# Kernel tuning notes

Hardware: AMD Instinct MI355X
Metric: run time of the kernel (lower is better)

## Reference

```python
import jax, jax.numpy as jnp
import numpy as np

N = 50000          # residues
E = 1000000        # edges
H = 128            # hidden_channels
CUT = 11.5         # cutoff
NR = 6             # num_radial
NS = 3             # num_spherical
NPE = 16           # num_pos_emb

def swish(x):
    return x * jax.nn.sigmoid(x)

def rbf(d):
    # Bessel-style radial basis with smooth cosine cutoff, [E, NR]
    u = jnp.clip(d / CUT, 0.0, 1.0)
    n = jnp.arange(1, NR + 1, dtype=jnp.float32)
    fc = 0.5 * (jnp.cos(jnp.pi * u) + 1.0)
    return jnp.sqrt(2.0 / CUT) * jnp.sin(n * jnp.pi * u[:, None]) / (d[:, None] + 1e-6) * fc[:, None]

def angle_emb(d, ang):
    # d_angle_emb: radial x cos(l*angle) -> [E, NR*NS]
    r = rbf(d)
    l = jnp.arange(NS, dtype=jnp.float32)
    a = jnp.cos(ang[:, None] * l)
    return (r[:, :, None] * a[:, None, :]).reshape(d.shape[0], NR * NS)

def theta_phi_emb(d, theta, phi):
    # d_theta_phi_emb: radial x angular(theta) x angular(phi) -> [E, NR*NS*NS]
    r = rbf(d)
    l = jnp.arange(NS, dtype=jnp.float32)
    ct = jnp.cos(theta[:, None] * l)
    cp = jnp.cos(phi[:, None] * l)
    return jnp.einsum('en,el,em->enlm', r, ct, cp).reshape(d.shape[0], NR * NS * NS)


def setup_inputs():
    key = jax.random.key(0)
    ks = jax.random.split(key, 20)
    f32 = jnp.float32
    pos = jax.random.normal(ks[0], (N, 3), f32) * 8.0
    pos_n = pos + jax.random.normal(ks[1], (N, 3), f32) * 0.8
    pos_c = pos + jax.random.normal(ks[2], (N, 3), f32) * 0.8
    z = jax.random.randint(ks[3], (N,), 0, 26)
    bb_embs = jax.random.normal(ks[4], (N, 6), f32)
    side_chain_embs = jax.random.normal(ks[5], (N, 8), f32)
    esm_embs = jax.random.normal(ks[6], (N, 1280), f32)
    batch = jnp.zeros((N,), jnp.int32)
    edge_index = jax.random.randint(ks[7], (2, E), 0, N)
    def w(k, shape):
        return jax.random.normal(k, shape, f32) * (1.0 / np.sqrt(shape[0]))
    edge_in = NR * NS * NS + 3 * NR * NS + NPE  # 54 + 54 + 16 = 124
    params = dict(
        W_emb=w(ks[8], (26 + 6 + 8, H // 2)), b_emb=jnp.zeros((H // 2,), f32),
        W_esm=w(ks[9], (1280, H // 2)), b_esm=jnp.zeros((H // 2,), f32),
        W_edge=w(ks[10], (edge_in, H)),
        W_msg=w(ks[11], (H, H)),
        W_upd=w(ks[12], (H, H)),
        W_o0=w(ks[13], (H, H)), b_o0=jnp.zeros((H,), f32),
        W_o1=w(ks[14], (H, 32)), b_o1=jnp.zeros((32,), f32),
        W_of=w(ks[15], (32, 1)), b_of=jnp.zeros((1,), f32),
        W_n0=w(ks[16], (H, 32)), b_n0=jnp.zeros((32,), f32),
        W_nf=w(ks[17], (32, 2)), b_nf=jnp.zeros((2,), f32),
    )
    return dict(z=z, pos=pos, pos_n=pos_n, pos_c=pos_c, bb_embs=bb_embs,
                side_chain_embs=side_chain_embs, esm_embs=esm_embs,
                batch=batch, edge_index=edge_index, **params)


def reference(z, pos, pos_n, pos_c, bb_embs, side_chain_embs, esm_embs, batch,
              edge_index, W_emb, b_emb, W_esm, b_esm, W_edge, W_msg, W_upd,
              W_o0, b_o0, W_o1, b_o1, W_of, b_of, W_n0, b_n0, W_nf, b_nf):
    # --- node embedding fusion (level='allatom+esm') ---
    oh = jax.nn.one_hot(z, 26, dtype=jnp.float32)
    x_a = jnp.concatenate([oh, bb_embs, side_chain_embs], axis=1) @ W_emb + b_emb
    x_s = esm_embs @ W_esm + b_esm
    x = jnp.concatenate([x_a, x_s], axis=-1)  # [N, H]

    j, i = edge_index[0], edge_index[1]

    # --- sinusoidal positional embedding of sequence offsets ---
    dpe = (j - i).astype(jnp.float32)
    freq = jnp.exp(jnp.arange(0, NPE, 2, dtype=jnp.float32) * (-np.log(10000.0) / NPE))
    ang = dpe[:, None] * freq
    pe = jnp.concatenate([jnp.cos(ang), jnp.sin(ang)], axis=-1)  # [E, NPE]

    # --- distance / theta / phi (triplet gathers via sequence neighbors) ---
    v_ji = pos[j] - pos[i]
    dist = jnp.linalg.norm(pos[i] - pos[j], axis=1)
    refi0 = (i - 1) % N
    refi1 = (i + 1) % N
    v_r0 = pos[refi0] - pos[i]
    v_r1 = pos[refi1] - pos[i]
    a = jnp.sum(v_ji * v_r0, axis=-1)
    b = jnp.linalg.norm(jnp.cross(v_ji, v_r0), axis=-1)
    theta = jnp.arctan2(b, a)
    p1 = jnp.cross(v_r0, v_r1)
    p2 = jnp.cross(v_r0, v_ji)
    a = jnp.sum(p1 * p2, axis=-1)
    b = jnp.sum(jnp.cross(p1, p2) * v_r0, axis=-1) / (jnp.linalg.norm(v_r0, axis=-1) + 1e-7)
    phi = jnp.arctan2(b, a)
    feature0 = theta_phi_emb(dist, theta, phi)  # [E, 54]

    # --- backbone-frame Euler angles (allatom branch) ---
    o1x = pos_n[i] - pos[i]
    o1z = jnp.cross(o1x, jnp.cross(o1x, pos_c[i] - pos[i]))
    o1zl = jnp.linalg.norm(o1z, axis=1) + 1e-7
    o2x = pos_n[j] - pos[j]
    o2z = jnp.cross(o2x, jnp.cross(o2x, pos_c[j] - pos[j]))
    o2zl = jnp.linalg.norm(o2z, axis=1) + 1e-7
    nvec = jnp.cross(o1z, o2z)
    angle1 = jnp.arctan2(jnp.sum(jnp.cross(o1x, nvec) * o1z, -1) / o1zl, jnp.sum(o1x * nvec, -1))
    angle2 = jnp.arctan2(jnp.linalg.norm(nvec, axis=-1), jnp.sum(o1z * o2z, -1))
    angle3 = jnp.arctan2(jnp.sum(jnp.cross(nvec, o2x) * o2z, -1) / o2zl, jnp.sum(nvec * o2x, -1))
    feature1 = jnp.concatenate([angle_emb(dist, angle1), angle_emb(dist, angle2),
                                angle_emb(dist, angle3)], axis=1)  # [E, 54]

    # --- message passing (gather-compute-scatter stand-in for model_E) ---
    ef = swish(jnp.concatenate([feature0, feature1, pe], axis=-1) @ W_edge)  # [E, H]
    m = swish(x[j] @ W_msg) * ef
    agg = jax.ops.segment_sum(m, i, num_segments=N)
    xe = x + swish(agg @ W_upd)

    # --- output heads (dropout inactive at inference) ---
    xn = jax.nn.relu(x @ W_n0 + b_n0)
    node_out = xn @ W_nf + b_nf                   # [N, 2]
    h = jax.nn.relu(xe @ W_o0 + b_o0)
    h = jax.nn.relu(h @ W_o1 + b_o1)
    out = jax.nn.sigmoid(h @ W_of + b_of)         # [N, 1]
    return out, node_out
```

## Files before the change

### kernel.cpp

```cpp
#include <hip/hip_runtime.h>
#include <math.h>
#include <stdint.h>

#define NRES 50000
#define NEDGE 1000000
#define PI_F 3.14159265358979323846f
#define NSEG 196

typedef __attribute__((ext_vector_type(8))) short short8;
typedef __attribute__((ext_vector_type(4))) float floatx4;
typedef __attribute__((ext_vector_type(2))) short bf16x2;
typedef __attribute__((address_space(1))) bf16x2* gbf16x2p;

struct f3 { float x, y, z; };
__device__ __forceinline__ f3 ld3(const float* __restrict__ p, int i) {
  return {p[3*i+0], p[3*i+1], p[3*i+2]};
}
__device__ __forceinline__ f3 f3sub(f3 a, f3 b){ return {a.x-b.x, a.y-b.y, a.z-b.z}; }
__device__ __forceinline__ f3 f3cross(f3 a, f3 b){
  return {a.y*b.z - a.z*b.y, a.z*b.x - a.x*b.z, a.x*b.y - a.y*b.x};
}
__device__ __forceinline__ float f3dot(f3 a, f3 b){ return a.x*b.x + a.y*b.y + a.z*b.z; }
__device__ __forceinline__ float swish_fast(float v){
  return v * __builtin_amdgcn_rcpf(1.0f + __expf(-v));
}
__device__ __forceinline__ short f2bf(float f){
  unsigned u = __float_as_uint(f);
  unsigned r = (u + 0x7fffu + ((u >> 16) & 1u)) >> 16;
  return (short)r;
}
__device__ __forceinline__ float bf2f(short s){
  return __uint_as_float(((unsigned)(unsigned short)s) << 16);
}
__device__ __forceinline__ float cos_atan2(float y, float x){
  return x * __builtin_amdgcn_rsqf(fmaxf(x*x + y*y, 1e-30f));
}
__device__ __forceinline__ void atom_pk_bf16(short* addr, bf16x2 v){
  __builtin_amdgcn_global_atomic_fadd_v2bf16((gbf16x2p)(uintptr_t)addr, v);
}

__device__ __forceinline__ void edge_features(
    int e, int j, int i,
    const float* __restrict__ pos, const float* __restrict__ posn,
    const float* __restrict__ posc, short (*sF)[136])
{
  f3 pj = ld3(pos, j), pi = ld3(pos, i);
  f3 vji = f3sub(pj, pi);
  float nji2 = f3dot(vji, vji);
  float dist = sqrtf(nji2);
  int r0i = (i == 0) ? (NRES - 1) : (i - 1);
  int r1i = (i == NRES - 1) ? 0 : (i + 1);
  f3 vr0 = f3sub(ld3(pos, r0i), pi);
  f3 vr1 = f3sub(ld3(pos, r1i), pi);
  float nr02 = f3dot(vr0, vr0);

  float ct = f3dot(vji, vr0) * __builtin_amdgcn_rsqf(fmaxf(nji2 * nr02, 1e-30f));
  f3 p1 = f3cross(vr0, vr1);
  f3 p2 = f3cross(vr0, vji);
  float pa = f3dot(p1, p2);
  float pb = f3dot(f3cross(p1, p2), vr0) / (sqrtf(nr02) + 1e-7f);
  float cp = cos_atan2(pb, pa);

  f3 pni = ld3(posn, i), pci = ld3(posc, i);
  f3 o1x = f3sub(pni, pi);
  f3 o1z = f3cross(o1x, f3cross(o1x, f3sub(pci, pi)));
  float no1z2 = f3dot(o1z, o1z);
  float o1zl = sqrtf(no1z2) + 1e-7f;
  f3 pnj = ld3(posn, j), pcj = ld3(posc, j);
  f3 o2x = f3sub(pnj, pj);
  f3 o2z = f3cross(o2x, f3cross(o2x, f3sub(pcj, pj)));
  float no2z2 = f3dot(o2z, o2z);
  float o2zl = sqrtf(no2z2) + 1e-7f;
  f3 nv = f3cross(o1z, o2z);
  float y1 = f3dot(f3cross(o1x, nv), o1z) / o1zl;
  float ca1 = cos_atan2(y1, f3dot(o1x, nv));
  float ca2 = f3dot(o1z, o2z) * __builtin_amdgcn_rsqf(fmaxf(no1z2 * no2z2, 1e-30f));
  float y3 = f3dot(f3cross(nv, o2x), o2z) / o2zl;
  float ca3 = cos_atan2(y3, f3dot(nv, o2x));

  float u = fminf(dist * (1.0f/11.5f), 1.0f);
  float spu, cpu;
  __sincosf(PI_F * u, &spu, &cpu);
  float fc = 0.5f * (cpu + 1.0f);
  float pref = 0.41702882811414954f * __builtin_amdgcn_rcpf(dist + 1e-6f) * fc;
  float rb[6];
  {
    float twoc = 2.0f * cpu;
    float s_nm1 = 0.0f, s_n = spu;
    #pragma unroll
    for (int nn = 0; nn < 6; ++nn) {
      rb[nn] = pref * s_n;
      float s_np1 = twoc * s_n - s_nm1;
      s_nm1 = s_n; s_n = s_np1;
    }
  }

  float ctv[3] = {1.0f, ct, 2.0f*ct*ct - 1.0f};
  float cpv[3] = {1.0f, cp, 2.0f*cp*cp - 1.0f};
  #pragma unroll
  for (int nn = 0; nn < 6; ++nn)
    #pragma unroll
    for (int l = 0; l < 3; ++l)
      #pragma unroll
      for (int m = 0; m < 3; ++m)
        sF[e][nn*9 + l*3 + m] = f2bf(rb[nn] * ctv[l] * cpv[m]);

  float cas[3] = {ca1, ca2, ca3};
  #pragma unroll
  for (int t = 0; t < 3; ++t) {
    float c = cas[t];
    float cav[3] = {1.0f, c, 2.0f*c*c - 1.0f};
    #pragma unroll
    for (int nn = 0; nn < 6; ++nn)
      #pragma unroll
      for (int l = 0; l < 3; ++l)
        sF[e][54 + t*18 + nn*3 + l] = f2bf(rb[nn] * cav[l]);
  }

  const float FRQ[8] = {1.0f, 0.31622776601683794f, 0.1f, 0.03162277660168379f,
                        0.01f, 0.003162277660168379f, 0.001f, 0.0003162277660168379f};
  float dpe = (float)(j - i);
  #pragma unroll
  for (int q = 0; q < 8; ++q) {
    float s, c;
    __sincosf(dpe * FRQ[q], &s, &c);
    sF[e][108 + q] = f2bf(c);
    sF[e][116 + q] = f2bf(s);
  }
  sF[e][124] = 0; sF[e][125] = 0; sF[e][126] = 0; sF[e][127] = 0;
}

__global__ __launch_bounds__(256) void k_wprep(
    const float* __restrict__ We, const float* __restrict__ Wm,
    const float* __restrict__ Ws, const float* __restrict__ Wu,
    const float* __restrict__ Wo0, const float* __restrict__ Wn0,
    const float* __restrict__ Wo1,
    short* __restrict__ Wef, short* __restrict__ Wmf, short* __restrict__ Wsf,
    short* __restrict__ Wuf, short* __restrict__ Wo0f,
    short* __restrict__ Wn0f, short* __restrict__ Wo1f)
{
  int gid = blockIdx.x * 256 + threadIdx.x;
  const float* src; short* dst; int NT, K, N, t;
  if      (gid < 16384)  { t = gid;          src = We;  dst = Wef;  NT = 8; K = 124;  N = 128; }
  else if (gid < 32768)  { t = gid - 16384;  src = Wm;  dst = Wmf;  NT = 8; K = 128;  N = 128; }
  else if (gid < 114688) { t = gid - 32768;  src = Ws;  dst = Wsf;  NT = 4; K = 1280; N = 64;  }
  else if (gid < 131072) { t = gid - 114688; src = Wu;  dst = Wuf;  NT = 8; K = 128;  N = 128; }
  else if (gid < 147456) { t = gid - 131072; src = Wo0; dst = Wo0f; NT = 8; K = 128;  N = 128; }
  else if (gid < 151552) { t = gid - 147456; src = Wn0; dst = Wn0f; NT = 2; K = 128;  N = 32;  }
  else if (gid < 155648) { t = gid - 151552; src = Wo1; dst = Wo1f; NT = 2; K = 128;  N = 32;  }
  else return;
  int j = t & 7, lane = (t >> 3) & 63;
  int rest = t >> 9;
  int nt = rest % NT, kt = rest / NT;
  int k = kt*32 + (lane >> 4)*8 + j, n = nt*16 + (lane & 15);
  dst[t] = f2bf((k < K) ? src[k*N + n] : 0.0f);
}

__global__ __launch_bounds__(256) void k_hist(
    const int* __restrict__ ei, int* __restrict__ bins)
{
  int e = blockIdx.x * 256 + threadIdx.x;
  if (e < NEDGE) atomicAdd(&bins[ei[NEDGE + e]], 1);
}

__global__ __launch_bounds__(256) void k_scan1(
    int* __restrict__ bins, int* __restrict__ bsum)
{
  __shared__ int s[256];
  const int t = threadIdx.x, b = blockIdx.x;
  const int idx = b * 256 + t;
  int v = (idx < NRES) ? bins[idx] : 0;
  s[t] = v;
  __syncthreads();
  #pragma unroll
  for (int d = 1; d < 256; d <<= 1) {
    int add = (t >= d) ? s[t - d] : 0;
    __syncthreads();
    if (t >= d) s[t] += add;
    __syncthreads();
  }
  if (idx < NRES) bins[idx] = s[t] - v;
  if (t == 255) bsum[b] = s[255];
}

__global__ __launch_bounds__(256) void k_scan2(int* __restrict__ bsum)
{
  __shared__ int s[256];
  const int t = threadIdx.x;
  int v = (t < NSEG) ? bsum[t] : 0;
  s[t] = v;
  __syncthreads();
  #pragma unroll
  for (int d = 1; d < 256; d <<= 1) {
    int add = (t >= d) ? s[t - d] : 0;
    __syncthreads();
    if (t >= d) s[t] += add;
    __syncthreads();
  }
  if (t < NSEG) bsum[t] = s[t] - v;
}

__global__ __launch_bounds__(256) void k_scan3(
    int* __restrict__ bins, const int* __restrict__ bsum)
{
  int idx = blockIdx.x * 256 + threadIdx.x;
  if (idx < NRES) bins[idx] += bsum[blockIdx.x];
}

__global__ __launch_bounds__(256) void k_scatter(
    const int* __restrict__ ei, int* __restrict__ bins, int* __restrict__ perm)
{
  int e = blockIdx.x * 256 + threadIdx.x;
  if (e < NEDGE) {
    int i = ei[NEDGE + e];
    int slot = atomicAdd(&bins[i], 1);
    if (slot >= 0 && slot < NEDGE) perm[slot] = e;
  }
}

__global__ __launch_bounds__(256) void k_xa(
    const int* __restrict__ z, const float* __restrict__ bb,
    const float* __restrict__ side, const float* __restrict__ W_emb,
    const float* __restrict__ b_emb, short* __restrict__ xb)
{
  int tid = threadIdx.x;
  int h = tid & 63;
  int n = blockIdx.x * 4 + (tid >> 6);
  if (n >= NRES) return;
  int zz = z[n];
  float acc = W_emb[zz * 64 + h] + b_emb[h];
  #pragma unroll
  for (int k = 0; k < 6; ++k) acc += bb[n*6 + k] * W_emb[(26 + k)*64 + h];
  #pragma unroll
  for (int k = 0; k < 8; ++k) acc += side[n*8 + k] * W_emb[(32 + k)*64 + h];
  xb[(size_t)n * 128 + h] = f2bf(acc);
}

__global__ __launch_bounds__(256) void k_esm(
    const float* __restrict__ esm, const short* __restrict__ Wsf,
    const float* __restrict__ b, short* __restrict__ xb)
{
  const int tid = threadIdx.x;
  const int lane = tid & 63, w = tid >> 6;
  const int quad = lane >> 4, colb = lane & 15;
  const int tile0 = blockIdx.x * 64 + w * 16;

  int arow = tile0 + colb;
  if (arow >= NRES) arow = NRES - 1;
  const float* ap = esm + (size_t)arow * 1280 + quad * 8;

  floatx4 acc[4];
  #pragma unroll
  for (int nt = 0; nt < 4; ++nt) acc[nt] = (floatx4){0.f, 0.f, 0.f, 0.f};

  for (int kt = 0; kt < 40; ++kt) {
    float4 v0 = *(const float4*)(ap + kt*32);
    float4 v1 = *(const float4*)(ap + kt*32 + 4);
    short8 a;
    a[0] = f2bf(v0.x); a[1] = f2bf(v0.y); a[2] = f2bf(v0.z); a[3] = f2bf(v0.w);
    a[4] = f2bf(v1.x); a[5] = f2bf(v1.y); a[6] = f2bf(v1.z); a[7] = f2bf(v1.w);
    #pragma unroll
    for (int nt = 0; nt < 4; ++nt) {
      short8 bf = *(const short8*)&Wsf[(size_t)((kt*4 + nt)*64 + lane)*8];
      acc[nt] = __builtin_amdgcn_mfma_f32_16x16x32_bf16(a, bf, acc[nt], 0, 0, 0);
    }
  }
  #pragma unroll
  for (int nt = 0; nt < 4; ++nt) {
    int ch = nt*16 + colb;
    float bias = b[ch];
    #pragma unroll
    for (int r = 0; r < 4; ++r) {
      int n = tile0 + quad*4 + r;
      if (n < NRES) xb[(size_t)n * 128 + 64 + ch] = f2bf(acc[nt][r] + bias);
    }
  }
}

__global__ __launch_bounds__(256) void k_msg(
    const short* __restrict__ xb, const short* __restrict__ Wmf,
    short* __restrict__ xmb)
{
  __shared__ __align__(16) short sX[64][136];
  __shared__ __align__(16) short sO[64][136];
  const int tid = threadIdx.x;
  const int lane = tid & 63, w = tid >> 6;
  const int quad = lane >> 4, colb = lane & 15;
  const int n0 = blockIdx.x * 64;

  #pragma unroll
  for (int it = 0; it < 4; ++it) {
    int idx = it * 256 + tid;
    int row = idx >> 4, c8 = idx & 15;
    int n = n0 + row;
    short8 v = (short8)(short)0;
    if (n < NRES) v = *(const short8*)&xb[(size_t)n * 128 + c8*8];
    *(short8*)&sX[row][c8*8] = v;
  }
  __syncthreads();

  floatx4 acc[4][2];
  #pragma unroll
  for (int mt = 0; mt < 4; ++mt) {
    acc[mt][0] = (floatx4){0.f,0.f,0.f,0.f};
    acc[mt][1] = (floatx4){0.f,0.f,0.f,0.f};
  }
  #pragma unroll
  for (int kt = 0; kt < 4; ++kt) {
    short8 b0 = *(const short8*)&Wmf[(size_t)((kt*8 + w*2 + 0)*64 + lane)*8];
    short8 b1 = *(const short8*)&Wmf[(size_t)((kt*8 + w*2 + 1)*64 + lane)*8];
    #pragma unroll
    for (int mt = 0; mt < 4; ++mt) {
      short8 a = *(const short8*)&sX[mt*16 + colb][kt*32 + quad*8];
      acc[mt][0] = __builtin_amdgcn_mfma_f32_16x16x32_bf16(a, b0, acc[mt][0], 0, 0, 0);
      acc[mt][1] = __builtin_amdgcn_mfma_f32_16x16x32_bf16(a, b1, acc[mt][1], 0, 0, 0);
    }
  }
  #pragma unroll
  for (int mt = 0; mt < 4; ++mt)
    #pragma unroll
    for (int nt = 0; nt < 2; ++nt)
      #pragma unroll
      for (int r = 0; r < 4; ++r)
        sO[mt*16 + quad*4 + r][w*32 + nt*16 + colb] = f2bf(swish_fast(acc[mt][nt][r]));
  __syncthreads();
  #pragma unroll
  for (int it = 0; it < 4; ++it) {
    int idx = it * 256 + tid;
    int row = idx >> 4, c8 = idx & 15;
    int n = n0 + row;
    if (n < NRES) *(short8*)&xmb[(size_t)n * 128 + c8*8] = *(short8*)&sO[row][c8*8];
  }
}

__global__ __launch_bounds__(256, 4) void k_edge_s(
    const int* __restrict__ perm, const int* __restrict__ ei,
    const float* __restrict__ pos,
    const float* __restrict__ posn, const float* __restrict__ posc,
    const short* __restrict__ xmb, const short* __restrict__ Wef,
    short* __restrict__ aggb)
{
  __shared__ int sJ[64];
  __shared__ int sI[64];
  __shared__ __align__(16) short sF[64][136];
  __shared__ __align__(16) short sXJ[64][136];

  const int tid = threadIdx.x;
  const int orig = blockIdx.x;
  const int xcd = orig & 7, sub = orig >> 3;
  const int wg = (xcd == 0 ? 0 : 1954 + (xcd - 1) * 1953) + sub;
  const int e0 = wg * 64;

  if (tid < 64) {
    int ep = perm[e0 + tid];
    ep = (ep < 0) ? 0 : ((ep >= NEDGE) ? NEDGE - 1 : ep);
    int jj = ei[ep], ii = ei[NEDGE + ep];
    sJ[tid] = (jj < 0) ? 0 : ((jj >= NRES) ? NRES - 1 : jj);
    sI[tid] = (ii < 0) ? 0 : ((ii >= NRES) ? NRES - 1 : ii);
  }
  __syncthreads();

  if (tid < 64) {
    edge_features(tid, sJ[tid], sI[tid], pos, posn, posc, sF);
  } else {
    const int t2 = tid - 64;
    for (int it = 0; it < 6; ++it) {
      int idx = it * 192 + t2;
      if (idx < 1024) {
        int row = idx >> 4;
        int c8 = idx & 15;
        *(short8*)&sXJ[row][c8*8] = *(const short8*)&xmb[(size_t)sJ[row] * 128 + c8*8];
      }
    }
  }
  __syncthreads();

  const int lane = tid & 63, w = tid >> 6;
  const int quad = lane >> 4, colb = lane & 15;
  const int nb = w * 2;

  short8 bE[4][2];
  #pragma unroll
  for (int kt = 0; kt < 4; ++kt)
    #pragma unroll
    for (int nt = 0; nt < 2; ++nt)
      bE[kt][nt] = *(const short8*)&Wef[(size_t)((kt*8 + nb + nt)*64 + lane)*8];

  floatx4 accE[4][2];
  #pragma unroll
  for (int mt = 0; mt < 4; ++mt) {
    accE[mt][0] = (floatx4){0.f, 0.f, 0.f, 0.f};
    accE[mt][1] = (floatx4){0.f, 0.f, 0.f, 0.f};
  }

  #pragma unroll
  for (int kt = 0; kt < 4; ++kt) {
    #pragma unroll
    for (int mt = 0; mt < 4; ++mt) {
      short8 af = *(const short8*)&sF[mt*16 + colb][kt*32 + quad*8];
      #pragma unroll
      for (int nt = 0; nt < 2; ++nt)
        accE[mt][nt] = __builtin_amdgcn_mfma_f32_16x16x32_bf16(af, bE[kt][nt], accE[mt][nt], 0, 0, 0);
    }
  }
  __syncthreads();

  short (*sM)[136] = sF;
  #pragma unroll
  for (int mt = 0; mt < 4; ++mt)
    #pragma unroll
    for (int nt = 0; nt < 2; ++nt) {
      int ch = w*32 + nt*16 + colb;
      #pragma unroll
      for (int r = 0; r < 4; ++r) {
        int e = mt*16 + quad*4 + r;
        float mv = bf2f(sXJ[e][ch]) * swish_fast(accE[mt][nt][r]);
        sM[e][ch] = f2bf(mv);
      }
    }
  __syncthreads();

  {
    const int p = tid & 63;
    const int g = tid >> 6;
    float ax = 0.f, ay = 0.f;
    int cur = sI[g * 16];
    #pragma unroll
    for (int rr = 0; rr < 16; ++rr) {
      int row = g * 16 + rr;
      int ii = sI[row];
      if (ii != cur) {
        bf16x2 v; v[0] = f2bf(ax); v[1] = f2bf(ay);
        atom_pk_bf16(&aggb[(size_t)cur * 128 + p*2], v);
        ax = 0.f; ay = 0.f; cur = ii;
      }
      bf16x2 mv = *(const bf16x2*)&sM[row][p*2];
      ax += bf2f(mv[0]); ay += bf2f(mv[1]);
    }
    bf16x2 v; v[0] = f2bf(ax); v[1] = f2bf(ay);
    atom_pk_bf16(&aggb[(size_t)cur * 128 + p*2], v);
  }
}

__global__ __launch_bounds__(256, 4) void k_edge_b(
    const int* __restrict__ ei, const float* __restrict__ pos,
    const float* __restrict__ posn, const float* __restrict__ posc,
    const short* __restrict__ xb, const short* __restrict__ Wef,
    const short* __restrict__ Wmf, short* __restrict__ aggb)
{
  __shared__ int sJ[64];
  __shared__ int sI[64];
  __shared__ __align__(16) short sF[64][136];
  __shared__ __align__(16) short sXJ[64][136];

  const int tid = threadIdx.x;
  const int e0 = blockIdx.x * 64;

  if (tid < 64) { sJ[tid] = ei[e0 + tid]; sI[tid] = ei[NEDGE + e0 + tid]; }
  __syncthreads();

  if (tid < 64) {
    edge_features(tid, sJ[tid], sI[tid], pos, posn, posc, sF);
  } else {
    const int t2 = tid - 64;
    for (int it = 0; it < 6; ++it) {
      int idx = it * 192 + t2;
      if (idx < 1024) {
        int row = idx >> 4;
        int c8 = idx & 15;
        *(short8*)&sXJ[row][c8*8] = *(const short8*)&xb[(size_t)sJ[row] * 128 + c8*8];
      }
    }
  }
  __syncthreads();

  const int lane = tid & 63, w = tid >> 6;
  const int quad = lane >> 4, colb = lane & 15;
  const int nb = w * 2;

  short8 bE[4][2], bM[4][2];
  #pragma unroll
  for (int kt = 0; kt < 4; ++kt)
    #pragma unroll
    for (int nt = 0; nt < 2; ++nt) {
      bE[kt][nt] = *(const short8*)&Wef[(size_t)((kt*8 + nb + nt)*64 + lane)*8];
      bM[kt][nt] = *(const short8*)&Wmf[(size_t)((kt*8 + nb + nt)*64 + lane)*8];
    }

  floatx4 accE[4][2], accM[4][2];
  #pragma unroll
  for (int mt = 0; mt < 4; ++mt)
    #pragma unroll
    for (int nt = 0; nt < 2; ++nt) {
      accE[mt][nt] = (floatx4){0.f, 0.f, 0.f, 0.f};
      accM[mt][nt] = (floatx4){0.f, 0.f, 0.f, 0.f};
    }

  #pragma unroll
  for (int kt = 0; kt < 4; ++kt) {
    #pragma unroll
    for (int mt = 0; mt < 4; ++mt) {
      short8 af = *(const short8*)&sF [mt*16 + colb][kt*32 + quad*8];
      short8 ax = *(const short8*)&sXJ[mt*16 + colb][kt*32 + quad*8];
      #pragma unroll
      for (int nt = 0; nt < 2; ++nt) {
        accE[mt][nt] = __builtin_amdgcn_mfma_f32_16x16x32_bf16(af, bE[kt][nt], accE[mt][nt], 0, 0, 0);
        accM[mt][nt] = __builtin_amdgcn_mfma_f32_16x16x32_bf16(ax, bM[kt][nt], accM[mt][nt], 0, 0, 0);
      }
    }
  }
  __syncthreads();

  short (*sM)[136] = sXJ;
  #pragma unroll
  for (int mt = 0; mt < 4; ++mt)
    #pragma unroll
    for (int nt = 0; nt < 2; ++nt) {
      int ch = w*32 + nt*16 + colb;
      #pragma unroll
      for (int r = 0; r < 4; ++r) {
        int e = mt*16 + quad*4 + r;
        sM[e][ch] = f2bf(swish_fast(accM[mt][nt][r]) * swish_fast(accE[mt][nt][r]));
      }
    }
  __syncthreads();

  #pragma unroll
  for (int it = 0; it < 16; ++it) {
    int flat = it * 256 + tid;
    int row = flat >> 6, p = flat & 63;
    bf16x2 v = *(const bf16x2*)&sM[row][p*2];
    atom_pk_bf16(&aggb[(size_t)sI[row] * 128 + p*2], v);
  }
}

__global__ __launch_bounds__(256) void k_upd(
    const short* __restrict__ xb, const short* __restrict__ aggb,
    const short* __restrict__ Wuf, const short* __restrict__ Wo0f,
    const short* __restrict__ Wn0f, const short* __restrict__ Wo1f,
    const float* __restrict__ bn0, const float* __restrict__ Wnf,
    const float* __restrict__ bnf, const float* __restrict__ bo0,
    const float* __restrict__ bo1, const float* __restrict__ Wof,
    const float* __restrict__ bof, float* __restrict__ out0,
    float* __restrict__ out1)
{
  __shared__ __align__(16) short sA[64][136];
  __shared__ __align__(16) short sX[64][136];
  __shared__ float sS[64][33];

  const int tid = threadIdx.x;
  const int lane = tid & 63, w = tid >> 6;
  const int quad = lane >> 4, colb = lane & 15;
  const int n0 = blockIdx.x * 64;

  #pragma unroll
  for (int it = 0; it < 4; ++it) {
    int idx = it * 256 + tid;
    int row = idx >> 4, c8 = idx & 15;
    int n = n0 + row;
    short8 va = (short8)(short)0, vx = (short8)(short)0;
    if (n < NRES) {
      va = *(const short8*)&aggb[(size_t)n * 128 + c8*8];
      vx = *(const short8*)&xb  [(size_t)n * 128 + c8*8];
    }
    *(short8*)&sA[row][c8*8] = va;
    *(short8*)&sX[row][c8*8] = vx;
  }
  __syncthreads();

  {
    floatx4 accN[2];
    accN[0] = (floatx4){0.f,0.f,0.f,0.f}; accN[1] = (floatx4){0.f,0.f,0.f,0.f};
    #pragma unroll
    for (int kt = 0; kt < 4; ++kt) {
      short8 a = *(const short8*)&sX[w*16 + colb][kt*32 + quad*8];
      #pragma unroll
      for (int nt = 0; nt < 2; ++nt) {
        short8 bf = *(const short8*)&Wn0f[(size_t)((kt*2 + nt)*64 + lane)*8];
        accN[nt] = __builtin_amdgcn_mfma_f32_16x16x32_bf16(a, bf, accN[nt], 0, 0, 0);
      }
    }
    #pragma unroll
    for (int nt = 0; nt < 2; ++nt) {
      int col = nt*16 + colb;
      float bias = bn0[col];
      #pragma unroll
      for (int r = 0; r < 4; ++r)
        sS[w*16 + quad*4 + r][col] = fmaxf(accN[nt][r] + bias, 0.0f);
    }
  }
  __syncthreads();
  if (tid < 128) {
    int row = tid >> 1, oc = tid & 1;
    int n = n0 + row;
    if (n < NRES) {
      float a2 = bnf[oc];
      #pragma unroll
      for (int k = 0; k < 32; ++k) a2 += sS[row][k] * Wnf[k*2 + oc];
      out1[(size_t)n * 2 + oc] = a2;
    }
  }

  floatx4 acc1[4][2];
  #pragma unroll
  for (int mt = 0; mt < 4; ++mt) {
    acc1[mt][0] = (floatx4){0.f,0.f,0.f,0.f};
    acc1[mt][1] = (floatx4){0.f,0.f,0.f,0.f};
  }
  #pragma unroll
  for (int kt = 0; kt < 4; ++kt) {
    short8 b0 = *(const short8*)&Wuf[(size_t)((kt*8 + w*2 + 0)*64 + lane)*8];
    short8 b1 = *(const short8*)&Wuf[(size_t)((kt*8 + w*2 + 1)*64 + lane)*8];
    #pragma unroll
    for (int mt = 0; mt < 4; ++mt) {
      short8 a = *(const short8*)&sA[mt*16 + colb][kt*32 + quad*8];
      acc1[mt][0] = __builtin_amdgcn_mfma_f32_16x16x32_bf16(a, b0, acc1[mt][0], 0, 0, 0);
      acc1[mt][1] = __builtin_amdgcn_mfma_f32_16x16x32_bf16(a, b1, acc1[mt][1], 0, 0, 0);
    }
  }
  __syncthreads();
  #pragma unroll
  for (int mt = 0; mt < 4; ++mt)
    #pragma unroll
    for (int nt = 0; nt < 2; ++nt)
      #pragma unroll
      for (int r = 0; r < 4; ++r) {
        int row = mt*16 + quad*4 + r, col = w*32 + nt*16 + colb;
        float xv = bf2f(sX[row][col]);
        sA[row][col] = f2bf(xv + swish_fast(acc1[mt][nt][r]));
      }
  __syncthreads();

  floatx4 acc2[4][2];
  #pragma unroll
  for (int mt = 0; mt < 4; ++mt) {
    acc2[mt][0] = (floatx4){0.f,0.f,0.f,0.f};
    acc2[mt][1] = (floatx4){0.f,0.f,0.f,0.f};
  }
  #pragma unroll
  for (int kt = 0; kt < 4; ++kt) {
    short8 b0 = *(const short8*)&Wo0f[(size_t)((kt*8 + w*2 + 0)*64 + lane)*8];
    short8 b1 = *(const short8*)&Wo0f[(size_t)((kt*8 + w*2 + 1)*64 + lane)*8];
    #pragma unroll
    for (int mt = 0; mt < 4; ++mt) {
      short8 a = *(const short8*)&sA[mt*16 + colb][kt*32 + quad*8];
      acc2[mt][0] = __builtin_amdgcn_mfma_f32_16x16x32_bf16(a, b0, acc2[mt][0], 0, 0, 0);
      acc2[mt][1] = __builtin_amdgcn_mfma_f32_16x16x32_bf16(a, b1, acc2[mt][1], 0, 0, 0);
    }
  }
  __syncthreads();
  #pragma unroll
  for (int mt = 0; mt < 4; ++mt)
    #pragma unroll
    for (int nt = 0; nt < 2; ++nt) {
      int col = w*32 + nt*16 + colb;
      float bias = bo0[col];
      #pragma unroll
      for (int r = 0; r < 4; ++r) {
        int row = mt*16 + quad*4 + r;
        sX[row][col] = f2bf(fmaxf(acc2[mt][nt][r] + bias, 0.0f));
      }
    }
  __syncthreads();

  {
    floatx4 accH[2];
    accH[0] = (floatx4){0.f,0.f,0.f,0.f}; accH[1] = (floatx4){0.f,0.f,0.f,0.f};
    #pragma unroll
    for (int kt = 0; kt < 4; ++kt) {
      short8 a = *(const short8*)&sX[w*16 + colb][kt*32 + quad*8];
      #pragma unroll
      for (int nt = 0; nt < 2; ++nt) {
        short8 bf = *(const short8*)&Wo1f[(size_t)((kt*2 + nt)*64 + lane)*8];
        accH[nt] = __builtin_amdgcn_mfma_f32_16x16x32_bf16(a, bf, accH[nt], 0, 0, 0);
      }
    }
    __syncthreads();
    #pragma unroll
    for (int nt = 0; nt < 2; ++nt) {
      int col = nt*16 + colb;
      float bias = bo1[col];
      #pragma unroll
      for (int r = 0; r < 4; ++r)
        sS[w*16 + quad*4 + r][col] = fmaxf(accH[nt][r] + bias, 0.0f);
    }
  }
  __syncthreads();

  if (tid < 64) {
    int n = n0 + tid;
    if (n < NRES) {
      float a2 = bof[0];
      #pragma unroll
      for (int k = 0; k < 32; ++k) a2 += sS[tid][k] * Wof[k];
      out0[n] = 1.0f / (1.0f + expf(-a2));
    }
  }
}

extern "C" void kernel_launch(void* const* d_in, const int* in_sizes, int n_in,
                              void* d_out, int out_size, void* d_ws, size_t ws_size,
                              hipStream_t stream) {
  (void)in_sizes; (void)n_in; (void)out_size;
  const int*   z     = (const int*)  d_in[0];
  const float* pos   = (const float*)d_in[1];
  const float* posn  = (const float*)d_in[2];
  const float* posc  = (const float*)d_in[3];
  const float* bb    = (const float*)d_in[4];
  const float* side  = (const float*)d_in[5];
  const float* esm   = (const float*)d_in[6];
  const int*   ei    = (const int*)  d_in[8];
  const float* W_emb = (const float*)d_in[9];
  const float* b_emb = (const float*)d_in[10];
  const float* W_esm = (const float*)d_in[11];
  const float* b_esm = (const float*)d_in[12];
  const float* W_edge= (const float*)d_in[13];
  const float* W_msg = (const float*)d_in[14];
  const float* W_upd = (const float*)d_in[15];
  const float* W_o0  = (const float*)d_in[16];
  const float* b_o0  = (const float*)d_in[17];
  const float* W_o1  = (const float*)d_in[18];
  const float* b_o1  = (const float*)d_in[19];
  const float* W_of  = (const float*)d_in[20];
  const float* b_of  = (const float*)d_in[21];
  const float* W_n0  = (const float*)d_in[22];
  const float* b_n0  = (const float*)d_in[23];
  const float* W_nf  = (const float*)d_in[24];
  const float* b_nf  = (const float*)d_in[25];

  float* out0 = (float*)d_out;
  float* out1 = out0 + NRES;
  char* ws = (char*)d_ws;

  const bool full = (ws_size >= (size_t)42912096);

  if (full) {
    short* xb   = (short*)ws;
    short* aggb = (short*)(ws + 12800000);
    short* xmb  = (short*)(ws + 25600000);
    short* Wef  = (short*)(ws + 38400000);
    short* Wmf  = (short*)(ws + 38432768);
    short* Wsf  = (short*)(ws + 38465536);
    short* Wuf  = (short*)(ws + 38629376);
    short* Wo0f = (short*)(ws + 38662144);
    short* Wn0f = (short*)(ws + 38694912);
    short* Wo1f = (short*)(ws + 38703104);
    int*   bins = (int*)  (ws + 38711296);
    int*   bsum = (int*)  (ws + 38911296);
    int*   perm = (int*)  (ws + 38912096);

    hipMemsetAsync(aggb, 0, (size_t)NRES * 128 * sizeof(short), stream);
    hipMemsetAsync(bins, 0, (size_t)NRES * sizeof(int), stream);

    k_wprep  <<<608, 256, 0, stream>>>(W_edge, W_msg, W_esm, W_upd, W_o0, W_n0, W_o1,
                                       Wef, Wmf, Wsf, Wuf, Wo0f, Wn0f, Wo1f);
    k_hist   <<<3907, 256, 0, stream>>>(ei, bins);
    k_scan1  <<<NSEG, 256, 0, stream>>>(bins, bsum);
    k_scan2  <<<1,    256, 0, stream>>>(bsum);
    k_scan3  <<<NSEG, 256, 0, stream>>>(bins, bsum);
    k_scatter<<<3907, 256, 0, stream>>>(ei, bins, perm);
    k_xa     <<<12500, 256, 0, stream>>>(z, bb, side, W_emb, b_emb, xb);
    k_esm    <<<782,   256, 0, stream>>>(esm, Wsf, b_esm, xb);
    k_msg    <<<782,   256, 0, stream>>>(xb, Wmf, xmb);
    k_edge_s <<<15625, 256, 0, stream>>>(perm, ei, pos, posn, posc, xmb, Wef, aggb);
    k_upd    <<<782,   256, 0, stream>>>(xb, aggb, Wuf, Wo0f, Wn0f, Wo1f,
                                         b_n0, W_nf, b_nf, b_o0, b_o1, W_of, b_of,
                                         out0, out1);
  } else {
    short* xb   = (short*)ws;
    short* aggb = (short*)(ws + 12800000);
    short* Wef  = (short*)(ws + 25600000);
    short* Wmf  = (short*)(ws + 25632768);
    short* Wsf  = (short*)(ws + 25665536);
    short* Wuf  = (short*)(ws + 25829376);
    short* Wo0f = (short*)(ws + 25862144);
    short* Wn0f = (short*)(ws + 25894912);
    short* Wo1f = (short*)(ws + 25903104);

    hipMemsetAsync(aggb, 0, (size_t)NRES * 128 * sizeof(short), stream);

    k_wprep <<<608, 256, 0, stream>>>(W_edge, W_msg, W_esm, W_upd, W_o0, W_n0, W_o1,
                                      Wef, Wmf, Wsf, Wuf, Wo0f, Wn0f, Wo1f);
    k_xa    <<<12500, 256, 0, stream>>>(z, bb, side, W_emb, b_emb, xb);
    k_esm   <<<782,   256, 0, stream>>>(esm, Wsf, b_esm, xb);
    k_edge_b<<<15625, 256, 0, stream>>>(ei, pos, posn, posc, xb, Wef, Wmf, aggb);
    k_upd   <<<782,   256, 0, stream>>>(xb, aggb, Wuf, Wo0f, Wn0f, Wo1f,
                                        b_n0, W_nf, b_nf, b_o0, b_o1, W_of, b_of,
                                        out0, out1);
  }
}
```

Measured before the change: 728.5 us.

## Fuse node embedding, ESM projection and message GEMM; store sorted edge pairs

Merges the three node kernels (atom embedding, ESM projection, message GEMM) into one k_node kernel that keeps the assembled x tile in shared memory instead of writing xb and reading it back. The scatter step now writes (j,i) pairs directly in sorted order, so the edge kernel no longer does a dependent gather through perm into edge_index. Edge-feature bf16 stores are packed two at a time with v_cvt_pk_bf16_f32. The workspace threshold for the full path rises by 4 MB, which may send smaller workspaces to the fallback path.

```diff
diff --git a/kernel.cpp b/kernel.cpp
--- a/kernel.cpp
+++ b/kernel.cpp
@@ -37,6 +37,11 @@
 }
 __device__ __forceinline__ void atom_pk_bf16(short* addr, bf16x2 v){
   __builtin_amdgcn_global_atomic_fadd_v2bf16((gbf16x2p)(uintptr_t)addr, v);
+}
+__device__ __forceinline__ unsigned pkbf(float lo, float hi){
+  unsigned r;
+  asm("v_cvt_pk_bf16_f32 %0, %1, %2" : "=v"(r) : "v"(lo), "v"(hi));
+  return r;
 }
 
 __device__ __forceinline__ void edge_features(
@@ -95,6 +100,7 @@
     }
   }
 
+  float pend = 0.0f;
   float ctv[3] = {1.0f, ct, 2.0f*ct*ct - 1.0f};
   float cpv[3] = {1.0f, cp, 2.0f*cp*cp - 1.0f};
   #pragma unroll
@@ -102,8 +108,12 @@
     #pragma unroll
     for (int l = 0; l < 3; ++l)
       #pragma unroll
-      for (int m = 0; m < 3; ++m)
-        sF[e][nn*9 + l*3 + m] = f2bf(rb[nn] * ctv[l] * cpv[m]);
+      for (int m = 0; m < 3; ++m) {
+        const int f = nn*9 + l*3 + m;
+        float v = rb[nn] * ctv[l] * cpv[m];
+        if (f & 1) *(unsigned*)&sF[e][f-1] = pkbf(pend, v);
+        else       pend = v;
+      }
 
   float cas[3] = {ca1, ca2, ca3};
   #pragma unroll
@@ -113,21 +123,27 @@
     #pragma unroll
     for (int nn = 0; nn < 6; ++nn)
       #pragma unroll
-      for (int l = 0; l < 3; ++l)
-        sF[e][54 + t*18 + nn*3 + l] = f2bf(rb[nn] * cav[l]);
+      for (int l = 0; l < 3; ++l) {
+        const int f = 54 + t*18 + nn*3 + l;
+        float v = rb[nn] * cav[l];
+        if (f & 1) *(unsigned*)&sF[e][f-1] = pkbf(pend, v);
+        else       pend = v;
+      }
   }
 
   const float FRQ[8] = {1.0f, 0.31622776601683794f, 0.1f, 0.03162277660168379f,
                         0.01f, 0.003162277660168379f, 0.001f, 0.0003162277660168379f};
   float dpe = (float)(j - i);
-  #pragma unroll
-  for (int q = 0; q < 8; ++q) {
-    float s, c;
-    __sincosf(dpe * FRQ[q], &s, &c);
-    sF[e][108 + q] = f2bf(c);
-    sF[e][116 + q] = f2bf(s);
-  }
-  sF[e][124] = 0; sF[e][125] = 0; sF[e][126] = 0; sF[e][127] = 0;
+  float cb[8], sb[8];
+  #pragma unroll
+  for (int q = 0; q < 8; ++q) __sincosf(dpe * FRQ[q], &sb[q], &cb[q]);
+  #pragma unroll
+  for (int q = 0; q < 8; q += 2) {
+    *(unsigned*)&sF[e][108 + q] = pkbf(cb[q], cb[q+1]);
+    *(unsigned*)&sF[e][116 + q] = pkbf(sb[q], sb[q+1]);
+  }
+  *(unsigned*)&sF[e][124] = 0u;
+  *(unsigned*)&sF[e][126] = 0u;
 }
 
 __global__ __launch_bounds__(256) void k_wprep(
@@ -208,13 +224,13 @@
 }
 
 __global__ __launch_bounds__(256) void k_scatter(
-    const int* __restrict__ ei, int* __restrict__ bins, int* __restrict__ perm)
+    const int* __restrict__ ei, int* __restrict__ bins, int2* __restrict__ sij)
 {
   int e = blockIdx.x * 256 + threadIdx.x;
   if (e < NEDGE) {
-    int i = ei[NEDGE + e];
+    int j = ei[e], i = ei[NEDGE + e];
     int slot = atomicAdd(&bins[i], 1);
-    if (slot >= 0 && slot < NEDGE) perm[slot] = e;
+    if (slot >= 0 && slot < NEDGE) sij[slot] = make_int2(j, i);
   }
 }
 
@@ -277,33 +293,93 @@
   }
 }
 
-__global__ __launch_bounds__(256) void k_msg(
-    const short* __restrict__ xb, const short* __restrict__ Wmf,
-    short* __restrict__ xmb)
+__global__ __launch_bounds__(256) void k_node(
+    const float* __restrict__ esm, const short* __restrict__ Wsf,
+    const float* __restrict__ b_esm,
+    const int* __restrict__ z, const float* __restrict__ bb,
+    const float* __restrict__ side, const float* __restrict__ W_emb,
+    const float* __restrict__ b_emb,
+    const short* __restrict__ Wmf,
+    short* __restrict__ xb, short* __restrict__ xmb)
 {
   __shared__ __align__(16) short sX[64][136];
-  __shared__ __align__(16) short sO[64][136];
+
   const int tid = threadIdx.x;
   const int lane = tid & 63, w = tid >> 6;
   const int quad = lane >> 4, colb = lane & 15;
   const int n0 = blockIdx.x * 64;
+  const int tile0 = n0 + w * 16;
+
+  int arow = tile0 + colb;
+  if (arow >= NRES) arow = NRES - 1;
+  const float* ap = esm + (size_t)arow * 1280 + quad * 8;
+
+  floatx4 acc[4];
+  #pragma unroll
+  for (int nt = 0; nt < 4; ++nt) acc[nt] = (floatx4){0.f, 0.f, 0.f, 0.f};
+
+  for (int kt = 0; kt < 40; ++kt) {
+    float4 v0 = *(const float4*)(ap + kt*32);
+    float4 v1 = *(const float4*)(ap + kt*32 + 4);
+    short8 a;
+    a[0] = f2bf(v0.x); a[1] = f2bf(v0.y); a[2] = f2bf(v0.z); a[3] = f2bf(v0.w);
+    a[4] = f2bf(v1.x); a[5] = f2bf(v1.y); a[6] = f2bf(v1.z); a[7] = f2bf(v1.w);
+    #pragma unroll
+    for (int nt = 0; nt < 4; ++nt) {
+      short8 bf = *(const short8*)&Wsf[(size_t)((kt*4 + nt)*64 + lane)*8];
+      acc[nt] = __builtin_amdgcn_mfma_f32_16x16x32_bf16(a, bf, acc[nt], 0, 0, 0);
+    }
+  }
+
+  #pragma unroll
+  for (int nt = 0; nt < 4; ++nt) {
+    int ch = nt*16 + colb;
+    float bias = b_esm[ch];
+    #pragma unroll
+    for (int r = 0; r < 4; ++r)
+      sX[w*16 + quad*4 + r][64 + ch] = f2bf(acc[nt][r] + bias);
+  }
+  {
+    int r2 = tid >> 2;
+    int n2 = n0 + r2; if (n2 >= NRES) n2 = NRES - 1;
+    int c0 = (tid & 3) * 16;
+    int zz = z[n2];
+    float bbv[6], sdv[8];
+    #pragma unroll
+    for (int k = 0; k < 6; ++k) bbv[k] = bb[n2*6 + k];
+    #pragma unroll
+    for (int k = 0; k < 8; ++k) sdv[k] = side[n2*8 + k];
+    #pragma unroll
+    for (int c = 0; c < 16; c += 2) {
+      float v0, v1;
+      #pragma unroll
+      for (int h = 0; h < 2; ++h) {
+        int col = c0 + c + h;
+        float a2 = W_emb[zz*64 + col] + b_emb[col];
+        #pragma unroll
+        for (int k = 0; k < 6; ++k) a2 += bbv[k] * W_emb[(26 + k)*64 + col];
+        #pragma unroll
+        for (int k = 0; k < 8; ++k) a2 += sdv[k] * W_emb[(32 + k)*64 + col];
+        if (h) v1 = a2; else v0 = a2;
+      }
+      *(unsigned*)&sX[r2][c0 + c] = pkbf(v0, v1);
+    }
+  }
+  __syncthreads();
 
   #pragma unroll
   for (int it = 0; it < 4; ++it) {
     int idx = it * 256 + tid;
     int row = idx >> 4, c8 = idx & 15;
     int n = n0 + row;
-    short8 v = (short8)(short)0;
-    if (n < NRES) v = *(const short8*)&xb[(size_t)n * 128 + c8*8];
-    *(short8*)&sX[row][c8*8] = v;
-  }
-  __syncthreads();
-
-  floatx4 acc[4][2];
+    if (n < NRES) *(short8*)&xb[(size_t)n * 128 + c8*8] = *(const short8*)&sX[row][c8*8];
+  }
+
+  floatx4 accM[4][2];
   #pragma unroll
   for (int mt = 0; mt < 4; ++mt) {
-    acc[mt][0] = (floatx4){0.f,0.f,0.f,0.f};
-    acc[mt][1] = (floatx4){0.f,0.f,0.f,0.f};
+    accM[mt][0] = (floatx4){0.f,0.f,0.f,0.f};
+    accM[mt][1] = (floatx4){0.f,0.f,0.f,0.f};
   }
   #pragma unroll
   for (int kt = 0; kt < 4; ++kt) {
@@ -312,29 +388,31 @@
     #pragma unroll
     for (int mt = 0; mt < 4; ++mt) {
       short8 a = *(const short8*)&sX[mt*16 + colb][kt*32 + quad*8];
-      acc[mt][0] = __builtin_amdgcn_mfma_f32_16x16x32_bf16(a, b0, acc[mt][0], 0, 0, 0);
-      acc[mt][1] = __builtin_amdgcn_mfma_f32_16x16x32_bf16(a, b1, acc[mt][1], 0, 0, 0);
-    }
-  }
+      accM[mt][0] = __builtin_amdgcn_mfma_f32_16x16x32_bf16(a, b0, accM[mt][0], 0, 0, 0);
+      accM[mt][1] = __builtin_amdgcn_mfma_f32_16x16x32_bf16(a, b1, accM[mt][1], 0, 0, 0);
+    }
+  }
+  __syncthreads();
+
   #pragma unroll
   for (int mt = 0; mt < 4; ++mt)
     #pragma unroll
     for (int nt = 0; nt < 2; ++nt)
       #pragma unroll
       for (int r = 0; r < 4; ++r)
-        sO[mt*16 + quad*4 + r][w*32 + nt*16 + colb] = f2bf(swish_fast(acc[mt][nt][r]));
+        sX[mt*16 + quad*4 + r][w*32 + nt*16 + colb] = f2bf(swish_fast(accM[mt][nt][r]));
   __syncthreads();
   #pragma unroll
   for (int it = 0; it < 4; ++it) {
     int idx = it * 256 + tid;
     int row = idx >> 4, c8 = idx & 15;
     int n = n0 + row;
-    if (n < NRES) *(short8*)&xmb[(size_t)n * 128 + c8*8] = *(short8*)&sO[row][c8*8];
+    if (n < NRES) *(short8*)&xmb[(size_t)n * 128 + c8*8] = *(const short8*)&sX[row][c8*8];
   }
 }
 
 __global__ __launch_bounds__(256, 4) void k_edge_s(
-    const int* __restrict__ perm, const int* __restrict__ ei,
+    const int2* __restrict__ sij,
     const float* __restrict__ pos,
     const float* __restrict__ posn, const float* __restrict__ posc,
     const short* __restrict__ xmb, const short* __restrict__ Wef,
@@ -352,9 +430,8 @@
   const int e0 = wg * 64;
 
   if (tid < 64) {
-    int ep = perm[e0 + tid];
-    ep = (ep < 0) ? 0 : ((ep >= NEDGE) ? NEDGE - 1 : ep);
-    int jj = ei[ep], ii = ei[NEDGE + ep];
+    int2 ji = sij[e0 + tid];
+    int jj = ji.x, ii = ji.y;
     sJ[tid] = (jj < 0) ? 0 : ((jj >= NRES) ? NRES - 1 : jj);
     sI[tid] = (ii < 0) ? 0 : ((ii >= NRES) ? NRES - 1 : ii);
   }
@@ -732,7 +809,7 @@
   float* out1 = out0 + NRES;
   char* ws = (char*)d_ws;
 
-  const bool full = (ws_size >= (size_t)42912096);
+  const bool full = (ws_size >= (size_t)46912096);
 
   if (full) {
     short* xb   = (short*)ws;
@@ -747,7 +824,7 @@
     short* Wo1f = (short*)(ws + 38703104);
     int*   bins = (int*)  (ws + 38711296);
     int*   bsum = (int*)  (ws + 38911296);
-    int*   perm = (int*)  (ws + 38912096);
+    int2*  sij  = (int2*) (ws + 38912096);
 
     hipMemsetAsync(aggb, 0, (size_t)NRES * 128 * sizeof(short), stream);
     hipMemsetAsync(bins, 0, (size_t)NRES * sizeof(int), stream);
@@ -758,11 +835,10 @@
     k_scan1  <<<NSEG, 256, 0, stream>>>(bins, bsum);
     k_scan2  <<<1,    256, 0, stream>>>(bsum);
     k_scan3  <<<NSEG, 256, 0, stream>>>(bins, bsum);
-    k_scatter<<<3907, 256, 0, stream>>>(ei, bins, perm);
-    k_xa     <<<12500, 256, 0, stream>>>(z, bb, side, W_emb, b_emb, xb);
-    k_esm    <<<782,   256, 0, stream>>>(esm, Wsf, b_esm, xb);
-    k_msg    <<<782,   256, 0, stream>>>(xb, Wmf, xmb);
-    k_edge_s <<<15625, 256, 0, stream>>>(perm, ei, pos, posn, posc, xmb, Wef, aggb);
+    k_scatter<<<3907, 256, 0, stream>>>(ei, bins, sij);
+    k_node   <<<782,  256, 0, stream>>>(esm, Wsf, b_esm, z, bb, side, W_emb, b_emb,
+                                        Wmf, xb, xmb);
+    k_edge_s <<<15625, 256, 0, stream>>>(sij, pos, posn, posc, xmb, Wef, aggb);
     k_upd    <<<782,   256, 0, stream>>>(xb, aggb, Wuf, Wo0f, Wn0f, Wo1f,
                                          b_n0, W_nf, b_nf, b_o0, b_o1, W_of, b_of,
                                          out0, out1);
```

Result: faster. 706.6 us (-3.0%).
